# Kernel optimization log

Measured on AMD Instinct MI355X. Metric: run time of the kernel, lower is better.

The kernel has to match this reference:

```python
import jax, jax.numpy as jnp
import numpy as np

H, HS, NH, T = 2048, 64, 32, 1024
DD, DA, DG, DV = 64, 64, 128, 32


def _ln(x, w, b, eps):
    mu = x.mean(-1, keepdims=True)
    var = ((x - mu) ** 2).mean(-1, keepdims=True)
    return (x - mu) / jnp.sqrt(var + eps) * w + b


def setup_inputs() -> dict:
    key = jax.random.key(0)
    ks = jax.random.split(key, 40)
    n = lambda i, shape, s=0.02: (jax.random.normal(ks[i], shape, jnp.float32) * s)
    u = lambda i, shape: jax.random.uniform(ks[i], shape, jnp.float32)
    return {
        'x': jax.random.normal(ks[0], (1, T, H), jnp.float32),
        'state1': jax.random.normal(ks[1], (1, H), jnp.float32),
        'state2': jnp.zeros((NH, HS, HS), jnp.float32),
        'v_first': jax.random.normal(ks[2], (1, T, H), jnp.float32),
        'x_r': u(3, (H,)), 'x_w': u(4, (H,)), 'x_k': u(5, (H,)),
        'x_v': u(6, (H,)), 'x_a': u(7, (H,)), 'x_g': u(8, (H,)),
        'W_r': n(9, (H, H)), 'W_k': n(10, (H, H)), 'W_v': n(11, (H, H)), 'W_o': n(12, (H, H)),
        'w0': n(13, (H,), 0.5) - 0.6,
        'w1': n(14, (H, DD)), 'w2': n(15, (DD, H)),
        'a0': jnp.zeros((H,), jnp.float32), 'a1': n(16, (H, DA)), 'a2': n(17, (DA, H)),
        'v0': jnp.zeros((H,), jnp.float32), 'v1': n(18, (H, DV)), 'v2': n(19, (DV, H)),
        'g1': n(20, (H, DG)), 'g2': n(21, (DG, H)),
        'k_k': n(22, (NH, HS), 0.5) + 1.0, 'k_a': n(23, (NH, HS), 0.5) + 1.0,
        'r_k': n(24, (NH, HS), 0.5),
        'ln_x_w': jnp.ones((H,), jnp.float32), 'ln_x_b': jnp.zeros((H,), jnp.float32),
        'ln1_w': jnp.ones((H,), jnp.float32), 'ln1_b': jnp.zeros((H,), jnp.float32),
    }


def reference(x, state1, state2, v_first, x_r, x_w, x_k, x_v, x_a, x_g,
              W_r, W_k, W_v, W_o, w0, w1, w2, a0, a1, a2, v0, v1, v2,
              g1, g2, k_k, k_a, r_k, ln_x_w, ln_x_b, ln1_w, ln1_b):
    T = x.shape[1]
    NH, HS = k_k.shape
    Hd = NH * HS
    last_x = x
    xn = _ln(x, ln1_w, ln1_b, 1e-5)
    # token shift: sx = shifted_past - x
    past = jnp.concatenate([state1[:, None, :], xn[:, :-1, :]], axis=1)
    sx = past - xn
    state1_out = xn[:, -1, :]
    xr = xn + x_r * sx
    xw = xn + x_w * sx
    xk = xn + x_k * sx
    xv = xn + x_v * sx
    xa = xn + x_a * sx
    xg = xn + x_g * sx
    r = xr @ W_r.T                                  # [1,T,H]
    k = (xk @ W_k.T).reshape(T, NH, HS)
    v = xv @ W_v.T                                  # [1,T,H]
    g = jax.nn.sigmoid(xg @ g1) @ g2                # gate
    a = jax.nn.sigmoid(a0 + (xa @ a1) @ a2).reshape(T, NH, HS)
    w = jnp.tanh(xw @ w1) @ w2                      # decay LoRA
    kk = k * k_k
    kk = kk / (jnp.linalg.norm(kk, axis=-1, keepdims=True) + 1e-12)
    k = k * (1.0 + (a - 1.0) * k_a)
    # layer_id != 0: v residual toward v_first
    v = v + (v_first - v) * jax.nn.sigmoid(v0 + (xv @ v1) @ v2)
    w = jnp.exp(-0.606531 * jax.nn.sigmoid(w0 + w)).reshape(T, NH, HS)
    b_seq = kk * a        # in-context addition direction
    a_seq = -kk           # removal direction
    r3 = r.reshape(T, NH, HS)
    v3 = v.reshape(T, NH, HS)

    def step(S, ts):
        w_t, k_t, v_t, a_t, b_t, r_t = ts          # each [NH,HS]
        S = S * w_t[:, None, :]                     # column-wise decay
        sa = jnp.einsum('hij,hj->hi', S, a_t)       # S @ a
        S = S + sa[:, :, None] * b_t[:, None, :] + v_t[:, :, None] * k_t[:, None, :]
        out = jnp.einsum('hij,hj->hi', S, r_t)      # S @ r
        return S, out

    state2_out, y = jax.lax.scan(step, state2, (w, k, v3, a_seq, b_seq, r3))  # y: [T,NH,HS]
    y = _ln(y, 1.0, 0.0, 0.00064)                   # GroupNorm-style per-head LN (no affine)
    y = y.reshape(1, T, Hd) * ln_x_w + ln_x_b
    bonus = ((r3 * k * r_k).sum(-1, keepdims=True) * v3).reshape(1, T, Hd)
    y = (y + bonus) * g
    y = y @ W_o.T
    return (last_x + y, state1_out, state2_out, v_first)
```

## Files before the change

### kernel.cpp

```cpp
#include <hip/hip_runtime.h>
#include <hip/hip_bf16.h>
#include <cstdint>
#include <cstddef>

#define T_TOK 1024
#define H_DIM 2048
#define NH 32
#define HS 64
#define TH (T_TOK * H_DIM)
#define HH (H_DIM * H_DIM)

using short8 = __attribute__((ext_vector_type(8))) short;
using f32x4  = __attribute__((ext_vector_type(4))) float;
typedef __hip_bfloat16 bf16;

__device__ __forceinline__ float sigmoidf_(float x) { return 1.0f / (1.0f + expf(-x)); }

__device__ __forceinline__ float wsum64(float v) {
#pragma unroll
    for (int m = 32; m; m >>= 1) v += __shfl_xor(v, m, 64);
    return v;
}

__device__ __forceinline__ float dpp_add16(float x) {
    int t;
    t = __builtin_amdgcn_update_dpp(0, __float_as_int(x), 0xB1, 0xF, 0xF, true);
    x += __int_as_float(t);
    t = __builtin_amdgcn_update_dpp(0, __float_as_int(x), 0x4E, 0xF, 0xF, true);
    x += __int_as_float(t);
    t = __builtin_amdgcn_update_dpp(0, __float_as_int(x), 0x141, 0xF, 0xF, true);
    x += __int_as_float(t);
    t = __builtin_amdgcn_update_dpp(0, __float_as_int(x), 0x140, 0xF, 0xF, true);
    x += __int_as_float(t);
    return x;
}

struct CastPar { const float* src[4]; bf16* dst[4]; };
__global__ __launch_bounds__(256) void castw_kernel(CastPar p) {
    int z = blockIdx.z;
    const float4* s = (const float4*)p.src[z];
    bf16* d = p.dst[z];
    int i = blockIdx.x * 256 + threadIdx.x;
    float4 v = s[i];
    int b = i * 4;
    d[b + 0] = __float2bfloat16(v.x);
    d[b + 1] = __float2bfloat16(v.y);
    d[b + 2] = __float2bfloat16(v.z);
    d[b + 3] = __float2bfloat16(v.w);
}

struct TPar { const float* src[8]; bf16* dst[8]; int R[8]; int C[8]; };
__global__ __launch_bounds__(256) void transpose_kernel(TPar p) {
    int z = blockIdx.z;
    int R = p.R[z], C = p.C[z];
    int e = blockIdx.x * 256 + threadIdx.x;
    if (e >= R * C) return;
    int r = e / C, c = e % C;
    p.dst[z][(size_t)c * R + r] = __float2bfloat16(p.src[z][e]);
}

__global__ __launch_bounds__(256) void ln_kernel(const float* __restrict__ x,
                                                 const float* __restrict__ w,
                                                 const float* __restrict__ b,
                                                 float* __restrict__ xn,
                                                 float* __restrict__ s1out) {
    int t = blockIdx.x, tid = threadIdx.x;
    const float* xt = x + (size_t)t * H_DIM;
    float v[8]; float s = 0.f, s2 = 0.f;
#pragma unroll
    for (int e = 0; e < 8; e++) { v[e] = xt[tid + 256 * e]; s += v[e]; s2 += v[e] * v[e]; }
    s = wsum64(s); s2 = wsum64(s2);
    __shared__ float ls[8];
    int wid = tid >> 6, ln = tid & 63;
    if (ln == 0) { ls[wid] = s; ls[4 + wid] = s2; }
    __syncthreads();
    s = ls[0] + ls[1] + ls[2] + ls[3];
    s2 = ls[4] + ls[5] + ls[6] + ls[7];
    float mu = s * (1.f / H_DIM);
    float var = s2 * (1.f / H_DIM) - mu * mu;
    float inv = rsqrtf(var + 1e-5f);
#pragma unroll
    for (int e = 0; e < 8; e++) {
        int h = tid + 256 * e;
        float o = (v[e] - mu) * inv * w[h] + b[h];
        xn[(size_t)t * H_DIM + h] = o;
        if (t == T_TOK - 1) s1out[h] = o;
    }
}

struct MixPar { const float* xn; const float* state1; const float* mv[6]; bf16* out[6]; };
__global__ __launch_bounds__(256) void mix_kernel(MixPar p) {
    int t = blockIdx.x, tid = threadIdx.x;
#pragma unroll
    for (int e = 0; e < 8; e++) {
        int h = tid + 256 * e;
        size_t idx = (size_t)t * H_DIM + h;
        float cur = p.xn[idx];
        float prev = (t == 0) ? p.state1[h] : p.xn[idx - H_DIM];
        float sx = prev - cur;
#pragma unroll
        for (int q = 0; q < 6; q++)
            p.out[q][idx] = __float2bfloat16(cur + p.mv[q][h] * sx);
    }
}

typedef const __attribute__((address_space(1))) uint32_t* gp1_t;
typedef __attribute__((address_space(3))) uint32_t* lp3_t;
__device__ __forceinline__ void async16(const bf16* g, short* l) {
    __builtin_amdgcn_global_load_lds((gp1_t)g, (lp3_t)l, 16, 0, 0);
}

struct BGPar { const bf16* X[4]; const bf16* W[4]; float* out[4]; const float* resid[4]; };
__global__ __launch_bounds__(256) void bgemm_kernel(BGPar p) {
    int z = blockIdx.z;
    const bf16* __restrict__ X = p.X[z];
    const bf16* __restrict__ W = p.W[z];
    float* __restrict__ out = p.out[z];
    const float* __restrict__ resid = p.resid[z];

    __shared__ short As[4][128 * 32];
    __shared__ short Bs[4][128 * 32];

    int m0 = blockIdx.y * 128, n0 = blockIdx.x * 128;
    int tid = threadIdx.x, lane = tid & 63, wv = tid >> 6;
    int m_off = (wv >> 1) * 64, n_off = (wv & 1) * 64;
    int lr = lane & 15, lq = lane >> 4;

    int srow = lane >> 2;
    int scol = (lane & 3) * 8;
    const bf16* Ag0 = X + (size_t)(m0 + wv * 32 + srow) * 2048 + scol;
    const bf16* Ag1 = Ag0 + (size_t)16 * 2048;
    const bf16* Bg0 = W + (size_t)(n0 + wv * 32 + srow) * 2048 + scol;
    const bf16* Bg1 = Bg0 + (size_t)16 * 2048;

    auto issue = [&](int at, int nb) {
        int kk = at * 32;
        async16(Ag0 + kk, &As[nb][(wv * 32) * 32]);
        async16(Ag1 + kk, &As[nb][(wv * 32 + 16) * 32]);
        async16(Bg0 + kk, &Bs[nb][(wv * 32) * 32]);
        async16(Bg1 + kk, &Bs[nb][(wv * 32 + 16) * 32]);
    };

    f32x4 acc[4][4];
#pragma unroll
    for (int a = 0; a < 4; a++)
#pragma unroll
        for (int b = 0; b < 4; b++)
#pragma unroll
            for (int r = 0; r < 4; r++) acc[a][b][r] = 0.f;

    issue(0, 0); issue(1, 1); issue(2, 2);

    for (int it = 0; it < 64; it++) {
        int nt = it + 3;
        int at = nt > 63 ? 63 : nt;
        issue(at, nt & 3);
        asm volatile("s_waitcnt vmcnt(12)" ::: "memory");
        asm volatile("s_barrier" ::: "memory");
        int buf = it & 3;
        short8 af[4], bfr[4];
#pragma unroll
        for (int mi = 0; mi < 4; mi++)
            af[mi] = *(const short8*)&As[buf][(m_off + mi * 16 + lr) * 32 + lq * 8];
#pragma unroll
        for (int ni = 0; ni < 4; ni++)
            bfr[ni] = *(const short8*)&Bs[buf][(n_off + ni * 16 + lr) * 32 + lq * 8];
#pragma unroll
        for (int mi = 0; mi < 4; mi++)
#pragma unroll
            for (int ni = 0; ni < 4; ni++)
                acc[mi][ni] = __builtin_amdgcn_mfma_f32_16x16x32_bf16(af[mi], bfr[ni], acc[mi][ni], 0, 0, 0);
        asm volatile("s_barrier" ::: "memory");
    }
    asm volatile("s_waitcnt vmcnt(0)" ::: "memory");

#pragma unroll
    for (int mi = 0; mi < 4; mi++)
#pragma unroll
        for (int ni = 0; ni < 4; ni++)
#pragma unroll
            for (int r = 0; r < 4; r++) {
                int rowg = m0 + m_off + mi * 16 + lq * 4 + r;
                int colg = n0 + n_off + ni * 16 + lr;
                size_t o = (size_t)rowg * 2048 + colg;
                float v = acc[mi][ni][r];
                if (resid) v += resid[o];
                out[o] = v;
            }
}

#define BM 128
#define BN 128
#define BK 32
#define LDK 40

__device__ __forceinline__ void gemm_core(const bf16* __restrict__ X, const bf16* __restrict__ W,
                                          int M, int N, int K, int act,
                                          const float* __restrict__ bias,
                                          float* __restrict__ outF, bf16* __restrict__ outB) {
    __shared__ short As[BM * LDK];
    __shared__ short Bs[BN * LDK];
    int m0 = blockIdx.y * BM, n0 = blockIdx.x * BN;
    if (n0 >= N) return;
    int tid = threadIdx.x;
    int lane = tid & 63, wid = tid >> 6;
    int m_off = (wid >> 1) * 64, n_off = (wid & 1) * 64;
    int lr = lane & 15, lq = lane >> 4;

    f32x4 acc[4][4];
#pragma unroll
    for (int a = 0; a < 4; a++)
#pragma unroll
        for (int b = 0; b < 4; b++)
#pragma unroll
            for (int r = 0; r < 4; r++) acc[a][b][r] = 0.f;

    for (int k0 = 0; k0 < K; k0 += BK) {
#pragma unroll
        for (int it = 0; it < 2; it++) {
            int c = tid + it * 256;
            int r = c >> 2;
            int cc = (c & 3) * 8;
            uint4 va = *(const uint4*)(X + (size_t)(m0 + r) * K + k0 + cc);
            *(uint4*)&As[r * LDK + cc] = va;
            uint4 vb;
            if (n0 + r < N) vb = *(const uint4*)(W + (size_t)(n0 + r) * K + k0 + cc);
            else            vb = make_uint4(0u, 0u, 0u, 0u);
            *(uint4*)&Bs[r * LDK + cc] = vb;
        }
        __syncthreads();
        short8 af[4], bfr[4];
#pragma unroll
        for (int mi = 0; mi < 4; mi++)
            af[mi] = *(const short8*)&As[(m_off + mi * 16 + lr) * LDK + lq * 8];
#pragma unroll
        for (int ni = 0; ni < 4; ni++)
            bfr[ni] = *(const short8*)&Bs[(n_off + ni * 16 + lr) * LDK + lq * 8];
#pragma unroll
        for (int mi = 0; mi < 4; mi++)
#pragma unroll
            for (int ni = 0; ni < 4; ni++)
                acc[mi][ni] = __builtin_amdgcn_mfma_f32_16x16x32_bf16(af[mi], bfr[ni], acc[mi][ni], 0, 0, 0);
        __syncthreads();
    }
#pragma unroll
    for (int mi = 0; mi < 4; mi++)
#pragma unroll
        for (int ni = 0; ni < 4; ni++)
#pragma unroll
            for (int r = 0; r < 4; r++) {
                int rowg = m0 + m_off + mi * 16 + lq * 4 + r;
                int colg = n0 + n_off + ni * 16 + lr;
                if (colg < N) {
                    float v = acc[mi][ni][r];
                    if (bias) v += bias[colg];
                    if (act == 1) v = sigmoidf_(v);
                    else if (act == 2) v = tanhf(v);
                    size_t o = (size_t)rowg * N + colg;
                    if (outF) outF[o] = v;
                    else      outB[o] = __float2bfloat16(v);
                }
            }
}

struct GPar {
    const bf16* X[4]; const bf16* W[4];
    float* outF[4]; bf16* outB[4];
    const float* bias[4];
    int N[4]; int K[4]; int act[4]; int M;
};
__global__ __launch_bounds__(256) void gemm_z_kernel(GPar p) {
    int z = blockIdx.z;
    gemm_core(p.X[z], p.W[z], p.M, p.N[z], p.K[z], p.act[z], p.bias[z], p.outF[z], p.outB[z]);
}

__global__ __launch_bounds__(64) void prep_kernel(float* __restrict__ k_io, float* __restrict__ v_io,
                                                  const float* __restrict__ v_first,
                                                  const float* __restrict__ vres,
                                                  float* __restrict__ w_io, float* __restrict__ a_io,
                                                  float* __restrict__ as_out,
                                                  const float* __restrict__ k_k,
                                                  const float* __restrict__ k_a,
                                                  const float* __restrict__ w0) {
    int h = blockIdx.x, t = blockIdx.y, i = threadIdx.x;
    int hi = h * HS + i;
    size_t idx = (size_t)t * H_DIM + hi;
    float kf = k_io[idx];
    float kk = kf * k_k[hi];
    float ss = wsum64(kk * kk);
    float kkn = kk / (sqrtf(ss) + 1e-12f);
    float a = a_io[idx];
    k_io[idx] = kf * (1.f + (a - 1.f) * k_a[hi]);
    float vv = v_io[idx];
    v_io[idx] = vv + (v_first[idx] - vv) * vres[idx];
    w_io[idx] = expf(-0.606531f * sigmoidf_(w0[hi] + w_io[idx]));
    a_io[idx] = kkn * a;
    as_out[idx] = -kkn;
}

struct SlotV { f32x4 w, a, b, k, r; float v; };

#define SCAN_ISSUE(sl, tt)                                                              \
    do {                                                                                \
        int tc_ = (tt) < T_TOK ? (tt) : T_TOK - 1;                                      \
        const float* wp_ = w_s + (size_t)tc_ * H_DIM + hb;                              \
        const float* ap_ = as_s + (size_t)tc_ * H_DIM + hb;                             \
        const float* bp_ = b_s + (size_t)tc_ * H_DIM + hb;                              \
        const float* kp_ = k_s + (size_t)tc_ * H_DIM + hb;                              \
        const float* rp_ = r_s + (size_t)tc_ * H_DIM + hb;                              \
        const float* vp_ = v_s + (size_t)tc_ * H_DIM + hb;                              \
        asm volatile("global_load_dwordx4 %0, %1, %2" : "=v"((sl).w) : "v"(jow), "s"(wp_)); \
        asm volatile("global_load_dwordx4 %0, %1, %2" : "=v"((sl).a) : "v"(jow), "s"(ap_)); \
        asm volatile("global_load_dwordx4 %0, %1, %2" : "=v"((sl).b) : "v"(jow), "s"(bp_)); \
        asm volatile("global_load_dwordx4 %0, %1, %2" : "=v"((sl).k) : "v"(jow), "s"(kp_)); \
        asm volatile("global_load_dwordx4 %0, %1, %2" : "=v"((sl).r) : "v"(jow), "s"(rp_)); \
        asm volatile("global_load_dword %0, %1, %2" : "=v"((sl).v) : "v"(rowoff), "s"(vp_)); \
    } while (0)

#define SCAN_PIN(sl)                                                                    \
    asm volatile("" : "+v"((sl).w), "+v"((sl).a), "+v"((sl).b), "+v"((sl).k),           \
                      "+v"((sl).r), "+v"((sl).v))

__device__ __forceinline__ void scan_compute(float S[4], const SlotV& s,
                                             const float* __restrict__ yp, int rowoff) {
    float sa = 0.f;
#pragma unroll
    for (int e = 0; e < 4; e++) { S[e] *= s.w[e]; sa = fmaf(S[e], s.a[e], sa); }
    sa = dpp_add16(sa);
    float o = 0.f;
#pragma unroll
    for (int e = 0; e < 4; e++) {
        S[e] = fmaf(sa, s.b[e], fmaf(s.v, s.k[e], S[e]));
        o = fmaf(S[e], s.r[e], o);
    }
    o = dpp_add16(o);
    asm volatile("global_store_dword %0, %1, %2" :: "v"(rowoff), "v"(o), "s"(yp) : "memory");
}

#define SCAN_STEP(d, t, W)                                                              \
    do {                                                                                \
        asm volatile("s_waitcnt vmcnt(" W ")");                                         \
        SCAN_PIN(sv[d]);                                                                \
        scan_compute(S, sv[d], y + (size_t)(t) * H_DIM + hb, rowoff);                   \
        SCAN_ISSUE(sv[d], (t) + 4);                                                     \
    } while (0)

__global__ __launch_bounds__(64) void scan_kernel(const float* __restrict__ w_s,
                                                  const float* __restrict__ k_s,
                                                  const float* __restrict__ v_s,
                                                  const float* __restrict__ as_s,
                                                  const float* __restrict__ b_s,
                                                  const float* __restrict__ r_s,
                                                  const float* __restrict__ s2in,
                                                  float* __restrict__ y,
                                                  float* __restrict__ s2out) {
    int h = blockIdx.x, q = blockIdx.y;
    int lane = threadIdx.x;
    int il = lane >> 4, jb = lane & 15;
    int row = q * 4 + il;
    int jo = jb * 4;
    int hb = h * HS;
    int jow = jo * 4;
    int rowoff = row * 4;

    float S[4];
    {
        const float* s0 = s2in + (size_t)h * HS * HS + (size_t)row * HS + jo;
        float4 t0 = *(const float4*)s0;
        S[0] = t0.x; S[1] = t0.y; S[2] = t0.z; S[3] = t0.w;
    }

    SlotV sv[4];
    SCAN_ISSUE(sv[0], 0);
    SCAN_ISSUE(sv[1], 1);
    SCAN_ISSUE(sv[2], 2);
    SCAN_ISSUE(sv[3], 3);

    SCAN_STEP(0, 0, "18");
    SCAN_STEP(1, 1, "19");
    SCAN_STEP(2, 2, "20");
    SCAN_STEP(3, 3, "21");
    for (int tb = 4; tb < T_TOK; tb += 4) {
        SCAN_STEP(0, tb + 0, "21");
        SCAN_STEP(1, tb + 1, "21");
        SCAN_STEP(2, tb + 2, "21");
        SCAN_STEP(3, tb + 3, "21");
    }
    asm volatile("s_waitcnt vmcnt(0)" ::: "memory");

    {
        float* so = s2out + (size_t)h * HS * HS + (size_t)row * HS + jo;
        float4 t0;
        t0.x = S[0]; t0.y = S[1]; t0.z = S[2]; t0.w = S[3];
        *(float4*)so = t0;
    }
}

__global__ __launch_bounds__(64) void post_kernel(const float* __restrict__ y,
                                                  const float* __restrict__ r_s,
                                                  const float* __restrict__ k_s,
                                                  const float* __restrict__ v_s,
                                                  const float* __restrict__ g_s,
                                                  const float* __restrict__ r_k,
                                                  const float* __restrict__ lnw,
                                                  const float* __restrict__ lnb,
                                                  bf16* __restrict__ ybig) {
    int h = blockIdx.x, t = blockIdx.y, i = threadIdx.x;
    int hi = h * HS + i;
    size_t idx = (size_t)t * H_DIM + hi;
    float yv = y[idx];
    float mu = wsum64(yv) * (1.f / HS);
    float d = yv - mu;
    float var = wsum64(d * d) * (1.f / HS);
    float yn = d * rsqrtf(var + 0.00064f);
    float bd = wsum64(r_s[idx] * k_s[idx] * r_k[hi]);
    float val = (yn * lnw[hi] + lnb[hi] + bd * v_s[idx]) * g_s[idx];
    ybig[idx] = __float2bfloat16(val);
}

extern "C" void kernel_launch(void* const* d_in, const int* in_sizes, int n_in,
                              void* d_out, int out_size, void* d_ws, size_t ws_size,
                              hipStream_t stream) {
    const float* x      = (const float*)d_in[0];
    const float* state1 = (const float*)d_in[1];
    const float* state2 = (const float*)d_in[2];
    const float* vfirst = (const float*)d_in[3];
    const float* x_r = (const float*)d_in[4];
    const float* x_w = (const float*)d_in[5];
    const float* x_k = (const float*)d_in[6];
    const float* x_v = (const float*)d_in[7];
    const float* x_a = (const float*)d_in[8];
    const float* x_g = (const float*)d_in[9];
    const float* W_r = (const float*)d_in[10];
    const float* W_k = (const float*)d_in[11];
    const float* W_v = (const float*)d_in[12];
    const float* W_o = (const float*)d_in[13];
    const float* w0 = (const float*)d_in[14];
    const float* w1 = (const float*)d_in[15];
    const float* w2 = (const float*)d_in[16];
    const float* a0 = (const float*)d_in[17];
    const float* a1 = (const float*)d_in[18];
    const float* a2 = (const float*)d_in[19];
    const float* v0 = (const float*)d_in[20];
    const float* v1 = (const float*)d_in[21];
    const float* v2 = (const float*)d_in[22];
    const float* g1 = (const float*)d_in[23];
    const float* g2 = (const float*)d_in[24];
    const float* k_k = (const float*)d_in[25];
    const float* k_a = (const float*)d_in[26];
    const float* r_k = (const float*)d_in[27];
    const float* ln_x_w = (const float*)d_in[28];
    const float* ln_x_b = (const float*)d_in[29];
    const float* ln1_w = (const float*)d_in[30];
    const float* ln1_b = (const float*)d_in[31];

    float* out0 = (float*)d_out;
    float* out1 = out0 + TH;
    float* out2 = out1 + H_DIM;
    float* out3 = out2 + NH * HS * HS;

    float* F = (float*)d_ws;
    float* xn   = F;
    float* as_s = F;
    float* rb   = F + (size_t)1 * TH;
    float* kb   = F + (size_t)2 * TH;
    float* vb   = F + (size_t)3 * TH;
    float* ab   = F + (size_t)4 * TH;
    float* wpre = F + (size_t)5 * TH;
    float* vresb= F + (size_t)6 * TH;
    float* gb   = F + (size_t)7 * TH;
    float* yb   = F + (size_t)8 * TH;
    bf16* B = (bf16*)(F + (size_t)9 * TH);
    bf16 *xrb = B, *xwb = B + (size_t)TH, *xkb = B + (size_t)2 * TH,
         *xvb = B + (size_t)3 * TH, *xab = B + (size_t)4 * TH, *xgb = B + (size_t)5 * TH;
    bf16* Wrb = B + (size_t)6 * TH;
    bf16* Wkb = Wrb + (size_t)HH;
    bf16* Wvb = Wkb + (size_t)HH;
    bf16* Wob = Wvb + (size_t)HH;
    bf16* pp = Wob + (size_t)HH;
    bf16* a1T = pp; pp += (size_t)H_DIM * 64;
    bf16* w1T = pp; pp += (size_t)H_DIM * 64;
    bf16* v1T = pp; pp += (size_t)H_DIM * 32;
    bf16* g1T = pp; pp += (size_t)H_DIM * 128;
    bf16* a2T = pp; pp += (size_t)H_DIM * 64;
    bf16* w2T = pp; pp += (size_t)H_DIM * 64;
    bf16* v2T = pp; pp += (size_t)H_DIM * 32;
    bf16* g2T = pp; pp += (size_t)H_DIM * 128;
    bf16* amid = pp; pp += (size_t)T_TOK * 64;
    bf16* wmid = pp; pp += (size_t)T_TOK * 64;
    bf16* vmid = pp; pp += (size_t)T_TOK * 32;
    bf16* gmid = pp; pp += (size_t)T_TOK * 128;
    bf16* ybig = pp; pp += (size_t)TH;

    CastPar cp;
    cp.src[0] = W_r; cp.src[1] = W_k; cp.src[2] = W_v; cp.src[3] = W_o;
    cp.dst[0] = Wrb; cp.dst[1] = Wkb; cp.dst[2] = Wvb; cp.dst[3] = Wob;
    castw_kernel<<<dim3(HH / 4 / 256, 1, 4), 256, 0, stream>>>(cp);

    TPar tp;
    tp.src[0] = a1; tp.dst[0] = a1T; tp.R[0] = H_DIM; tp.C[0] = 64;
    tp.src[1] = w1; tp.dst[1] = w1T; tp.R[1] = H_DIM; tp.C[1] = 64;
    tp.src[2] = v1; tp.dst[2] = v1T; tp.R[2] = H_DIM; tp.C[2] = 32;
    tp.src[3] = g1; tp.dst[3] = g1T; tp.R[3] = H_DIM; tp.C[3] = 128;
    tp.src[4] = a2; tp.dst[4] = a2T; tp.R[4] = 64;  tp.C[4] = H_DIM;
    tp.src[5] = w2; tp.dst[5] = w2T; tp.R[5] = 64;  tp.C[5] = H_DIM;
    tp.src[6] = v2; tp.dst[6] = v2T; tp.R[6] = 32;  tp.C[6] = H_DIM;
    tp.src[7] = g2; tp.dst[7] = g2T; tp.R[7] = 128; tp.C[7] = H_DIM;
    transpose_kernel<<<dim3((H_DIM * 128 + 255) / 256, 1, 8), 256, 0, stream>>>(tp);

    ln_kernel<<<dim3(T_TOK), 256, 0, stream>>>(x, ln1_w, ln1_b, xn, out1);

    MixPar mp; mp.xn = xn; mp.state1 = state1;
    mp.mv[0] = x_r; mp.mv[1] = x_w; mp.mv[2] = x_k; mp.mv[3] = x_v; mp.mv[4] = x_a; mp.mv[5] = x_g;
    mp.out[0] = xrb; mp.out[1] = xwb; mp.out[2] = xkb; mp.out[3] = xvb; mp.out[4] = xab; mp.out[5] = xgb;
    mix_kernel<<<dim3(T_TOK), 256, 0, stream>>>(mp);

    BGPar bp{};
    bp.X[0] = xrb; bp.W[0] = Wrb; bp.out[0] = rb; bp.resid[0] = nullptr;
    bp.X[1] = xkb; bp.W[1] = Wkb; bp.out[1] = kb; bp.resid[1] = nullptr;
    bp.X[2] = xvb; bp.W[2] = Wvb; bp.out[2] = vb; bp.resid[2] = nullptr;
    bgemm_kernel<<<dim3(16, 8, 3), 256, 0, stream>>>(bp);

    GPar s1{}; s1.M = T_TOK;
    s1.X[0] = xab; s1.W[0] = a1T; s1.outB[0] = amid; s1.N[0] = 64;  s1.K[0] = H_DIM; s1.act[0] = 0;
    s1.X[1] = xwb; s1.W[1] = w1T; s1.outB[1] = wmid; s1.N[1] = 64;  s1.K[1] = H_DIM; s1.act[1] = 2;
    s1.X[2] = xvb; s1.W[2] = v1T; s1.outB[2] = vmid; s1.N[2] = 32;  s1.K[2] = H_DIM; s1.act[2] = 0;
    s1.X[3] = xgb; s1.W[3] = g1T; s1.outB[3] = gmid; s1.N[3] = 128; s1.K[3] = H_DIM; s1.act[3] = 1;
    gemm_z_kernel<<<dim3(1, 8, 4), 256, 0, stream>>>(s1);

    GPar s2{}; s2.M = T_TOK;
    s2.X[0] = amid; s2.W[0] = a2T; s2.outF[0] = ab;    s2.N[0] = H_DIM; s2.K[0] = 64;  s2.act[0] = 1; s2.bias[0] = a0;
    s2.X[1] = wmid; s2.W[1] = w2T; s2.outF[1] = wpre;  s2.N[1] = H_DIM; s2.K[1] = 64;  s2.act[1] = 0;
    s2.X[2] = vmid; s2.W[2] = v2T; s2.outF[2] = vresb; s2.N[2] = H_DIM; s2.K[2] = 32;  s2.act[2] = 1; s2.bias[2] = v0;
    s2.X[3] = gmid; s2.W[3] = g2T; s2.outF[3] = gb;    s2.N[3] = H_DIM; s2.K[3] = 128; s2.act[3] = 0;
    gemm_z_kernel<<<dim3(16, 8, 4), 256, 0, stream>>>(s2);

    prep_kernel<<<dim3(NH, T_TOK), 64, 0, stream>>>(kb, vb, vfirst, vresb, wpre, ab, as_s, k_k, k_a, w0);

    scan_kernel<<<dim3(NH, 16), 64, 0, stream>>>(wpre, kb, vb, as_s, ab, rb, state2, yb, out2);

    post_kernel<<<dim3(NH, T_TOK), 64, 0, stream>>>(yb, rb, kb, vb, gb, r_k, ln_x_w, ln_x_b, ybig);

    BGPar bo{};
    bo.X[0] = ybig; bo.W[0] = Wob; bo.out[0] = out0; bo.resid[0] = x;
    bgemm_kernel<<<dim3(16, 8, 1), 256, 0, stream>>>(bo);

    hipMemcpyAsync(out3, (const void*)vfirst, (size_t)TH * sizeof(float),
                   hipMemcpyDeviceToDevice, stream);
}
```

Baseline: 569.2 us.

## Unify GEMMs into async-pipelined kernel, tile transpose, and software-pipeline scan steps

Replaces the plain LDS-staged small GEMM with the async 4-stage pipelined GEMM, generalized over N, K, activation, bias and residual, so the LoRA-style projections also use global_load_lds prefetching. The weight transpose now goes through a 32x32 shared-memory tile so both reads and writes are coalesced. The scan loop is restructured to defer the output reduction of step t into step t+1, pairing the two DPP reductions so they interleave and shorten the serial dependency chain. A slack buffer is added after ybig, apparently to cover loads past the end of row-padded inputs when the small-N GEMM reads W rows beyond N.

```diff
diff --git a/kernel.cpp b/kernel.cpp
--- a/kernel.cpp
+++ b/kernel.cpp
@@ -33,6 +33,22 @@
     t = __builtin_amdgcn_update_dpp(0, __float_as_int(x), 0x140, 0xF, 0xF, true);
     x += __int_as_float(t);
     return x;
+}
+
+__device__ __forceinline__ void dpp_add16_pair(float& x, float& y) {
+    int tx, ty;
+    tx = __builtin_amdgcn_update_dpp(0, __float_as_int(x), 0xB1, 0xF, 0xF, true);
+    ty = __builtin_amdgcn_update_dpp(0, __float_as_int(y), 0xB1, 0xF, 0xF, true);
+    x += __int_as_float(tx); y += __int_as_float(ty);
+    tx = __builtin_amdgcn_update_dpp(0, __float_as_int(x), 0x4E, 0xF, 0xF, true);
+    ty = __builtin_amdgcn_update_dpp(0, __float_as_int(y), 0x4E, 0xF, 0xF, true);
+    x += __int_as_float(tx); y += __int_as_float(ty);
+    tx = __builtin_amdgcn_update_dpp(0, __float_as_int(x), 0x141, 0xF, 0xF, true);
+    ty = __builtin_amdgcn_update_dpp(0, __float_as_int(y), 0x141, 0xF, 0xF, true);
+    x += __int_as_float(tx); y += __int_as_float(ty);
+    tx = __builtin_amdgcn_update_dpp(0, __float_as_int(x), 0x140, 0xF, 0xF, true);
+    ty = __builtin_amdgcn_update_dpp(0, __float_as_int(y), 0x140, 0xF, 0xF, true);
+    x += __int_as_float(tx); y += __int_as_float(ty);
 }
 
 struct CastPar { const float* src[4]; bf16* dst[4]; };
@@ -53,10 +69,23 @@
 __global__ __launch_bounds__(256) void transpose_kernel(TPar p) {
     int z = blockIdx.z;
     int R = p.R[z], C = p.C[z];
-    int e = blockIdx.x * 256 + threadIdx.x;
-    if (e >= R * C) return;
-    int r = e / C, c = e % C;
-    p.dst[z][(size_t)c * R + r] = __float2bfloat16(p.src[z][e]);
+    int tC = (C + 31) >> 5;
+    int tR = (R + 31) >> 5;
+    if (blockIdx.x >= tC * tR) return;
+    int r0 = (blockIdx.x / tC) * 32, c0 = (blockIdx.x % tC) * 32;
+    __shared__ bf16 tl[32][33];
+    int tx = threadIdx.x & 31, ty = threadIdx.x >> 5;
+#pragma unroll
+    for (int k = 0; k < 4; k++) {
+        int r = r0 + ty + k * 8, c = c0 + tx;
+        if (r < R && c < C) tl[ty + k * 8][tx] = __float2bfloat16(p.src[z][(size_t)r * C + c]);
+    }
+    __syncthreads();
+#pragma unroll
+    for (int k = 0; k < 4; k++) {
+        int r = r0 + tx, c = c0 + ty + k * 8;
+        if (r < R && c < C) p.dst[z][(size_t)c * R + r] = tl[tx][ty + k * 8];
+    }
 }
 
 __global__ __launch_bounds__(256) void ln_kernel(const float* __restrict__ x,
@@ -110,13 +139,21 @@
     __builtin_amdgcn_global_load_lds((gp1_t)g, (lp3_t)l, 16, 0, 0);
 }
 
-struct BGPar { const bf16* X[4]; const bf16* W[4]; float* out[4]; const float* resid[4]; };
-__global__ __launch_bounds__(256) void bgemm_kernel(BGPar p) {
+struct UGPar {
+    const bf16* X[4]; const bf16* W[4];
+    float* outF[4]; bf16* outB[4];
+    const float* bias[4]; const float* resid[4];
+    int N[4]; int K[4]; int act[4];
+};
+__global__ __launch_bounds__(256) void ugemm_kernel(UGPar p) {
     int z = blockIdx.z;
     const bf16* __restrict__ X = p.X[z];
     const bf16* __restrict__ W = p.W[z];
-    float* __restrict__ out = p.out[z];
+    int N = p.N[z], K = p.K[z], act = p.act[z];
+    const float* __restrict__ bias = p.bias[z];
     const float* __restrict__ resid = p.resid[z];
+    float* __restrict__ outF = p.outF[z];
+    bf16* __restrict__ outB = p.outB[z];
 
     __shared__ short As[4][128 * 32];
     __shared__ short Bs[4][128 * 32];
@@ -128,13 +165,14 @@
 
     int srow = lane >> 2;
     int scol = (lane & 3) * 8;
-    const bf16* Ag0 = X + (size_t)(m0 + wv * 32 + srow) * 2048 + scol;
-    const bf16* Ag1 = Ag0 + (size_t)16 * 2048;
-    const bf16* Bg0 = W + (size_t)(n0 + wv * 32 + srow) * 2048 + scol;
-    const bf16* Bg1 = Bg0 + (size_t)16 * 2048;
-
-    auto issue = [&](int at, int nb) {
-        int kk = at * 32;
+    const bf16* Ag0 = X + (size_t)(m0 + wv * 32 + srow) * K + scol;
+    const bf16* Ag1 = Ag0 + (size_t)16 * K;
+    const bf16* Bg0 = W + (size_t)(n0 + wv * 32 + srow) * K + scol;
+    const bf16* Bg1 = Bg0 + (size_t)16 * K;
+
+    int stages = K >> 5;
+    auto issue = [&](int tile, int nb) {
+        int kk = tile * 32;
         async16(Ag0 + kk, &As[nb][(wv * 32) * 32]);
         async16(Ag1 + kk, &As[nb][(wv * 32 + 16) * 32]);
         async16(Bg0 + kk, &Bs[nb][(wv * 32) * 32]);
@@ -149,11 +187,13 @@
 #pragma unroll
             for (int r = 0; r < 4; r++) acc[a][b][r] = 0.f;
 
-    issue(0, 0); issue(1, 1); issue(2, 2);
-
-    for (int it = 0; it < 64; it++) {
+    issue(0, 0);
+    issue(1 < stages ? 1 : stages - 1, 1);
+    issue(2 < stages ? 2 : stages - 1, 2);
+
+    for (int it = 0; it < stages; it++) {
         int nt = it + 3;
-        int at = nt > 63 ? 63 : nt;
+        int at = nt < stages ? nt : stages - 1;
         issue(at, nt & 3);
         asm volatile("s_waitcnt vmcnt(12)" ::: "memory");
         asm volatile("s_barrier" ::: "memory");
@@ -174,75 +214,6 @@
     }
     asm volatile("s_waitcnt vmcnt(0)" ::: "memory");
 
-#pragma unroll
-    for (int mi = 0; mi < 4; mi++)
-#pragma unroll
-        for (int ni = 0; ni < 4; ni++)
-#pragma unroll
-            for (int r = 0; r < 4; r++) {
-                int rowg = m0 + m_off + mi * 16 + lq * 4 + r;
-                int colg = n0 + n_off + ni * 16 + lr;
-                size_t o = (size_t)rowg * 2048 + colg;
-                float v = acc[mi][ni][r];
-                if (resid) v += resid[o];
-                out[o] = v;
-            }
-}
-
-#define BM 128
-#define BN 128
-#define BK 32
-#define LDK 40
-
-__device__ __forceinline__ void gemm_core(const bf16* __restrict__ X, const bf16* __restrict__ W,
-                                          int M, int N, int K, int act,
-                                          const float* __restrict__ bias,
-                                          float* __restrict__ outF, bf16* __restrict__ outB) {
-    __shared__ short As[BM * LDK];
-    __shared__ short Bs[BN * LDK];
-    int m0 = blockIdx.y * BM, n0 = blockIdx.x * BN;
-    if (n0 >= N) return;
-    int tid = threadIdx.x;
-    int lane = tid & 63, wid = tid >> 6;
-    int m_off = (wid >> 1) * 64, n_off = (wid & 1) * 64;
-    int lr = lane & 15, lq = lane >> 4;
-
-    f32x4 acc[4][4];
-#pragma unroll
-    for (int a = 0; a < 4; a++)
-#pragma unroll
-        for (int b = 0; b < 4; b++)
-#pragma unroll
-            for (int r = 0; r < 4; r++) acc[a][b][r] = 0.f;
-
-    for (int k0 = 0; k0 < K; k0 += BK) {
-#pragma unroll
-        for (int it = 0; it < 2; it++) {
-            int c = tid + it * 256;
-            int r = c >> 2;
-            int cc = (c & 3) * 8;
-            uint4 va = *(const uint4*)(X + (size_t)(m0 + r) * K + k0 + cc);
-            *(uint4*)&As[r * LDK + cc] = va;
-            uint4 vb;
-            if (n0 + r < N) vb = *(const uint4*)(W + (size_t)(n0 + r) * K + k0 + cc);
-            else            vb = make_uint4(0u, 0u, 0u, 0u);
-            *(uint4*)&Bs[r * LDK + cc] = vb;
-        }
-        __syncthreads();
-        short8 af[4], bfr[4];
-#pragma unroll
-        for (int mi = 0; mi < 4; mi++)
-            af[mi] = *(const short8*)&As[(m_off + mi * 16 + lr) * LDK + lq * 8];
-#pragma unroll
-        for (int ni = 0; ni < 4; ni++)
-            bfr[ni] = *(const short8*)&Bs[(n_off + ni * 16 + lr) * LDK + lq * 8];
-#pragma unroll
-        for (int mi = 0; mi < 4; mi++)
-#pragma unroll
-            for (int ni = 0; ni < 4; ni++)
-                acc[mi][ni] = __builtin_amdgcn_mfma_f32_16x16x32_bf16(af[mi], bfr[ni], acc[mi][ni], 0, 0, 0);
-        __syncthreads();
-    }
 #pragma unroll
     for (int mi = 0; mi < 4; mi++)
 #pragma unroll
@@ -257,21 +228,11 @@
                     if (act == 1) v = sigmoidf_(v);
                     else if (act == 2) v = tanhf(v);
                     size_t o = (size_t)rowg * N + colg;
+                    if (resid) v += resid[o];
                     if (outF) outF[o] = v;
                     else      outB[o] = __float2bfloat16(v);
                 }
             }
-}
-
-struct GPar {
-    const bf16* X[4]; const bf16* W[4];
-    float* outF[4]; bf16* outB[4];
-    const float* bias[4];
-    int N[4]; int K[4]; int act[4]; int M;
-};
-__global__ __launch_bounds__(256) void gemm_z_kernel(GPar p) {
-    int z = blockIdx.z;
-    gemm_core(p.X[z], p.W[z], p.M, p.N[z], p.K[z], p.act[z], p.bias[z], p.outF[z], p.outB[z]);
 }
 
 __global__ __launch_bounds__(64) void prep_kernel(float* __restrict__ k_io, float* __restrict__ v_io,
@@ -321,27 +282,31 @@
     asm volatile("" : "+v"((sl).w), "+v"((sl).a), "+v"((sl).b), "+v"((sl).k),           \
                       "+v"((sl).r), "+v"((sl).v))
 
-__device__ __forceinline__ void scan_compute(float S[4], const SlotV& s,
-                                             const float* __restrict__ yp, int rowoff) {
-    float sa = 0.f;
-#pragma unroll
-    for (int e = 0; e < 4; e++) { S[e] *= s.w[e]; sa = fmaf(S[e], s.a[e], sa); }
-    sa = dpp_add16(sa);
-    float o = 0.f;
-#pragma unroll
-    for (int e = 0; e < 4; e++) {
-        S[e] = fmaf(sa, s.b[e], fmaf(s.v, s.k[e], S[e]));
-        o = fmaf(S[e], s.r[e], o);
-    }
-    o = dpp_add16(o);
-    asm volatile("global_store_dword %0, %1, %2" :: "v"(rowoff), "v"(o), "s"(yp) : "memory");
-}
-
 #define SCAN_STEP(d, t, W)                                                              \
     do {                                                                                \
         asm volatile("s_waitcnt vmcnt(" W ")");                                         \
         SCAN_PIN(sv[d]);                                                                \
-        scan_compute(S, sv[d], y + (size_t)(t) * H_DIM + hb, rowoff);                   \
+        float Sw0 = S[0] * sv[d].w[0], Sw1 = S[1] * sv[d].w[1];                         \
+        float Sw2 = S[2] * sv[d].w[2], Sw3 = S[3] * sv[d].w[3];                         \
+        float pA = Sw0 * sv[d].a[0], pB = Sw2 * sv[d].a[2];                             \
+        pA = fmaf(Sw1, sv[d].a[1], pA); pB = fmaf(Sw3, sv[d].a[3], pB);                 \
+        float sa = pA + pB;                                                             \
+        float pre0 = fmaf(sv[d].v, sv[d].k[0], Sw0);                                    \
+        float pre1 = fmaf(sv[d].v, sv[d].k[1], Sw1);                                    \
+        float pre2 = fmaf(sv[d].v, sv[d].k[2], Sw2);                                    \
+        float pre3 = fmaf(sv[d].v, sv[d].k[3], Sw3);                                    \
+        dpp_add16_pair(sa, ov);                                                         \
+        {                                                                               \
+            const float* yp_ = y + (size_t)((t) - 1) * H_DIM + hb;                      \
+            asm volatile("global_store_dword %0, %1, %2" :: "v"(rowoff), "v"(ov), "s"(yp_) : "memory"); \
+        }                                                                               \
+        S[0] = fmaf(sa, sv[d].b[0], pre0);                                              \
+        S[1] = fmaf(sa, sv[d].b[1], pre1);                                              \
+        S[2] = fmaf(sa, sv[d].b[2], pre2);                                              \
+        S[3] = fmaf(sa, sv[d].b[3], pre3);                                              \
+        float qA = S[0] * sv[d].r[0], qB = S[2] * sv[d].r[2];                           \
+        qA = fmaf(S[1], sv[d].r[1], qA); qB = fmaf(S[3], sv[d].r[3], qB);               \
+        ov = qA + qB;                                                                   \
         SCAN_ISSUE(sv[d], (t) + 4);                                                     \
     } while (0)
 
@@ -376,15 +341,41 @@
     SCAN_ISSUE(sv[2], 2);
     SCAN_ISSUE(sv[3], 3);
 
-    SCAN_STEP(0, 0, "18");
-    SCAN_STEP(1, 1, "19");
-    SCAN_STEP(2, 2, "20");
-    SCAN_STEP(3, 3, "21");
+    float ov;
+    {
+        asm volatile("s_waitcnt vmcnt(18)");
+        SCAN_PIN(sv[0]);
+        float Sw0 = S[0] * sv[0].w[0], Sw1 = S[1] * sv[0].w[1];
+        float Sw2 = S[2] * sv[0].w[2], Sw3 = S[3] * sv[0].w[3];
+        float pA = Sw0 * sv[0].a[0], pB = Sw2 * sv[0].a[2];
+        pA = fmaf(Sw1, sv[0].a[1], pA); pB = fmaf(Sw3, sv[0].a[3], pB);
+        float sa = dpp_add16(pA + pB);
+        float pre0 = fmaf(sv[0].v, sv[0].k[0], Sw0);
+        float pre1 = fmaf(sv[0].v, sv[0].k[1], Sw1);
+        float pre2 = fmaf(sv[0].v, sv[0].k[2], Sw2);
+        float pre3 = fmaf(sv[0].v, sv[0].k[3], Sw3);
+        S[0] = fmaf(sa, sv[0].b[0], pre0);
+        S[1] = fmaf(sa, sv[0].b[1], pre1);
+        S[2] = fmaf(sa, sv[0].b[2], pre2);
+        S[3] = fmaf(sa, sv[0].b[3], pre3);
+        float qA = S[0] * sv[0].r[0], qB = S[2] * sv[0].r[2];
+        qA = fmaf(S[1], sv[0].r[1], qA); qB = fmaf(S[3], sv[0].r[3], qB);
+        ov = qA + qB;
+        SCAN_ISSUE(sv[0], 4);
+    }
+    SCAN_STEP(1, 1, "18");
+    SCAN_STEP(2, 2, "19");
+    SCAN_STEP(3, 3, "20");
     for (int tb = 4; tb < T_TOK; tb += 4) {
         SCAN_STEP(0, tb + 0, "21");
         SCAN_STEP(1, tb + 1, "21");
         SCAN_STEP(2, tb + 2, "21");
         SCAN_STEP(3, tb + 3, "21");
+    }
+    {
+        float o = dpp_add16(ov);
+        const float* yp_ = y + (size_t)(T_TOK - 1) * H_DIM + hb;
+        asm volatile("global_store_dword %0, %1, %2" :: "v"(rowoff), "v"(o), "s"(yp_) : "memory");
     }
     asm volatile("s_waitcnt vmcnt(0)" ::: "memory");
 
@@ -491,6 +482,8 @@
     bf16* vmid = pp; pp += (size_t)T_TOK * 32;
     bf16* gmid = pp; pp += (size_t)T_TOK * 128;
     bf16* ybig = pp; pp += (size_t)TH;
+    bf16* slack = pp; pp += (size_t)128 * H_DIM;
+    (void)slack;
 
     CastPar cp;
     cp.src[0] = W_r; cp.src[1] = W_k; cp.src[2] = W_v; cp.src[3] = W_o;
@@ -506,7 +499,7 @@
     tp.src[5] = w2; tp.dst[5] = w2T; tp.R[5] = 64;  tp.C[5] = H_DIM;
     tp.src[6] = v2; tp.dst[6] = v2T; tp.R[6] = 32;  tp.C[6] = H_DIM;
     tp.src[7] = g2; tp.dst[7] = g2T; tp.R[7] = 128; tp.C[7] = H_DIM;
-    transpose_kernel<<<dim3((H_DIM * 128 + 255) / 256, 1, 8), 256, 0, stream>>>(tp);
+    transpose_kernel<<<dim3(256, 1, 8), 256, 0, stream>>>(tp);
 
     ln_kernel<<<dim3(T_TOK), 256, 0, stream>>>(x, ln1_w, ln1_b, xn, out1);
 
@@ -515,25 +508,25 @@
     mp.out[0] = xrb; mp.out[1] = xwb; mp.out[2] = xkb; mp.out[3] = xvb; mp.out[4] = xab; mp.out[5] = xgb;
     mix_kernel<<<dim3(T_TOK), 256, 0, stream>>>(mp);
 
-    BGPar bp{};
-    bp.X[0] = xrb; bp.W[0] = Wrb; bp.out[0] = rb; bp.resid[0] = nullptr;
-    bp.X[1] = xkb; bp.W[1] = Wkb; bp.out[1] = kb; bp.resid[1] = nullptr;
-    bp.X[2] = xvb; bp.W[2] = Wvb; bp.out[2] = vb; bp.resid[2] = nullptr;
-    bgemm_kernel<<<dim3(16, 8, 3), 256, 0, stream>>>(bp);
-
-    GPar s1{}; s1.M = T_TOK;
+    UGPar gp{};
+    gp.X[0] = xrb; gp.W[0] = Wrb; gp.outF[0] = rb; gp.N[0] = H_DIM; gp.K[0] = H_DIM;
+    gp.X[1] = xkb; gp.W[1] = Wkb; gp.outF[1] = kb; gp.N[1] = H_DIM; gp.K[1] = H_DIM;
+    gp.X[2] = xvb; gp.W[2] = Wvb; gp.outF[2] = vb; gp.N[2] = H_DIM; gp.K[2] = H_DIM;
+    ugemm_kernel<<<dim3(16, 8, 3), 256, 0, stream>>>(gp);
+
+    UGPar s1{};
     s1.X[0] = xab; s1.W[0] = a1T; s1.outB[0] = amid; s1.N[0] = 64;  s1.K[0] = H_DIM; s1.act[0] = 0;
     s1.X[1] = xwb; s1.W[1] = w1T; s1.outB[1] = wmid; s1.N[1] = 64;  s1.K[1] = H_DIM; s1.act[1] = 2;
     s1.X[2] = xvb; s1.W[2] = v1T; s1.outB[2] = vmid; s1.N[2] = 32;  s1.K[2] = H_DIM; s1.act[2] = 0;
     s1.X[3] = xgb; s1.W[3] = g1T; s1.outB[3] = gmid; s1.N[3] = 128; s1.K[3] = H_DIM; s1.act[3] = 1;
-    gemm_z_kernel<<<dim3(1, 8, 4), 256, 0, stream>>>(s1);
-
-    GPar s2{}; s2.M = T_TOK;
+    ugemm_kernel<<<dim3(1, 8, 4), 256, 0, stream>>>(s1);
+
+    UGPar s2{};
     s2.X[0] = amid; s2.W[0] = a2T; s2.outF[0] = ab;    s2.N[0] = H_DIM; s2.K[0] = 64;  s2.act[0] = 1; s2.bias[0] = a0;
     s2.X[1] = wmid; s2.W[1] = w2T; s2.outF[1] = wpre;  s2.N[1] = H_DIM; s2.K[1] = 64;  s2.act[1] = 0;
     s2.X[2] = vmid; s2.W[2] = v2T; s2.outF[2] = vresb; s2.N[2] = H_DIM; s2.K[2] = 32;  s2.act[2] = 1; s2.bias[2] = v0;
     s2.X[3] = gmid; s2.W[3] = g2T; s2.outF[3] = gb;    s2.N[3] = H_DIM; s2.K[3] = 128; s2.act[3] = 0;
-    gemm_z_kernel<<<dim3(16, 8, 4), 256, 0, stream>>>(s2);
+    ugemm_kernel<<<dim3(16, 8, 4), 256, 0, stream>>>(s2);
 
     prep_kernel<<<dim3(NH, T_TOK), 64, 0, stream>>>(kb, vb, vfirst, vresb, wpre, ab, as_s, k_k, k_a, w0);
 
@@ -541,9 +534,9 @@
 
     post_kernel<<<dim3(NH, T_TOK), 64, 0, stream>>>(yb, rb, kb, vb, gb, r_k, ln_x_w, ln_x_b, ybig);
 
-    BGPar bo{};
-    bo.X[0] = ybig; bo.W[0] = Wob; bo.out[0] = out0; bo.resid[0] = x;
-    bgemm_kernel<<<dim3(16, 8, 1), 256, 0, stream>>>(bo);
+    UGPar go{};
+    go.X[0] = ybig; go.W[0] = Wob; go.outF[0] = out0; go.N[0] = H_DIM; go.K[0] = H_DIM; go.resid[0] = x;
+    ugemm_kernel<<<dim3(16, 8, 1), 256, 0, stream>>>(go);
 
     hipMemcpyAsync(out3, (const void*)vfirst, (size_t)TH * sizeof(float),
                    hipMemcpyDeviceToDevice, stream);
```

Result: slower. 627.3 us (+10.2%).
